# Performance work log

Measured on AMD Instinct MI355X. Metric: run time of the kernel, lower is better.

## Reference

```python
import jax, jax.numpy as jnp
import numpy as np

B, N, NPOINT, NSAMPLE = 8, 8192, 512, 32
D, NHEAD, NLAYERS, DIM_OUT = 128, 8, 4, 256
HD = D // NHEAD
DFF = 2 * D
EPS = 1e-5

_gather = jax.vmap(lambda p, i: p[i])  # p: [N,C], i: [...] -> [...,C]


def _ln(x, g, b):
    m = jnp.mean(x, -1, keepdims=True)
    v = jnp.var(x, -1, keepdims=True)
    return (x - m) / jnp.sqrt(v + EPS) * g + b


def _fps(pts):
    # pts: [B,N,3] -> centroid indices [B,NPOINT]; start index 0 (torch uses randint)
    Bb, Nn, _ = pts.shape
    def step(carry, _):
        dist, far = carry
        cen = jax.vmap(lambda p, f: p[f])(pts, far)[:, None, :]  # [B,1,3]
        dist = jnp.minimum(dist, jnp.sum((pts - cen) ** 2, -1))
        return (dist, jnp.argmax(dist, -1)), far
    init = (jnp.full((Bb, Nn), 1e10, pts.dtype), jnp.zeros((Bb,), jnp.int32))
    _, cents = jax.lax.scan(step, init, None, length=NPOINT)
    return cents.T  # [B,NPOINT]


def _interp_linear(x, n_out):
    # x: [B,C,S] -> [B,C,n_out], linear, align_corners=True
    S = x.shape[-1]
    pos = jnp.arange(n_out) * ((S - 1) / (n_out - 1))
    i0 = jnp.floor(pos).astype(jnp.int32)
    i1 = jnp.minimum(i0 + 1, S - 1)
    w = (pos - i0).astype(x.dtype)
    return x[..., i0] * (1 - w) + x[..., i1] * w


def _layer(x, p):
    wqkv, bqkv, wo, bo, g1, be1, w1, bf1, w2, bf2, g2, be2 = p
    Bt, K, _ = x.shape
    qkv = x @ wqkv.T + bqkv
    q, k, v = jnp.split(qkv, 3, axis=-1)
    q = q.reshape(Bt, K, NHEAD, HD)
    k = k.reshape(Bt, K, NHEAD, HD)
    v = v.reshape(Bt, K, NHEAD, HD)
    att = jax.nn.softmax(jnp.einsum('bqhd,bkhd->bhqk', q, k) / jnp.sqrt(jnp.float32(HD)), axis=-1)
    o = jnp.einsum('bhqk,bkhd->bqhd', att, v).reshape(Bt, K, D)
    x = _ln(x + o @ wo.T + bo, g1, be1)
    ff = jax.nn.relu(x @ w1.T + bf1) @ w2.T + bf2
    return _ln(x + ff, g2, be2)


def setup_inputs():
    key = jax.random.key(0)
    ks = jax.random.split(key, 10)
    w = lambda k, s: jax.random.normal(k, s, jnp.float32) * 0.02
    return {
        'xyz': jax.random.normal(ks[0], (B, 3, N), jnp.float32),
        'features': jax.random.normal(ks[1], (B, D, N), jnp.float32),
        'pe_w1': w(ks[2], (D // 2, 3)), 'pe_b1': jnp.zeros((D // 2,), jnp.float32),
        'bn_gamma': jnp.ones((D // 2,), jnp.float32), 'bn_beta': jnp.zeros((D // 2,), jnp.float32),
        'bn_mean': jnp.zeros((D // 2,), jnp.float32), 'bn_var': jnp.ones((D // 2,), jnp.float32),
        'pe_w2': w(ks[3], (D, D // 2)), 'pe_b2': jnp.zeros((D,), jnp.float32),
        'attn_wqkv': w(ks[4], (NLAYERS, 3 * D, D)), 'attn_bqkv': jnp.zeros((NLAYERS, 3 * D), jnp.float32),
        'attn_wo': w(ks[5], (NLAYERS, D, D)), 'attn_bo': jnp.zeros((NLAYERS, D), jnp.float32),
        'ln1_g': jnp.ones((NLAYERS, D), jnp.float32), 'ln1_b': jnp.zeros((NLAYERS, D), jnp.float32),
        'ffn_w1': w(ks[6], (NLAYERS, DFF, D)), 'ffn_b1': jnp.zeros((NLAYERS, DFF), jnp.float32),
        'ffn_w2': w(ks[7], (NLAYERS, D, DFF)), 'ffn_b2': jnp.zeros((NLAYERS, D), jnp.float32),
        'ln2_g': jnp.ones((NLAYERS, D), jnp.float32), 'ln2_b': jnp.zeros((NLAYERS, D), jnp.float32),
        'fc_w': w(ks[8], (DIM_OUT, D)), 'fc_b': jnp.zeros((DIM_OUT,), jnp.float32),
    }


def reference(xyz, features, pe_w1, pe_b1, bn_gamma, bn_beta, bn_mean, bn_var, pe_w2, pe_b2,
              attn_wqkv, attn_bqkv, attn_wo, attn_bo, ln1_g, ln1_b,
              ffn_w1, ffn_b1, ffn_w2, ffn_b2, ln2_g, ln2_b, fc_w, fc_b):
    pts = jnp.transpose(xyz, (0, 2, 1))                 # [B,N,3]
    fps_idx = _fps(pts)                                 # [B,S]
    new_xyz = _gather(pts, fps_idx)                     # [B,S,3]
    # kNN: squared distances [B,S,N]
    d2 = (jnp.sum(new_xyz ** 2, -1)[..., None] + jnp.sum(pts ** 2, -1)[:, None, :]
          - 2.0 * jnp.einsum('bsc,bnc->bsn', new_xyz, pts))
    _, gidx = jax.lax.top_k(-d2, NSAMPLE)               # [B,S,K]
    gxyz = _gather(pts, gidx)                           # [B,S,K,3]
    gfeat = _gather(jnp.transpose(features, (0, 2, 1)), gidx)  # [B,S,K,D]
    # positional encoding: 1x1 conv -> BN (eval) -> relu -> 1x1 conv
    h = gxyz @ pe_w1.T + pe_b1
    h = (h - bn_mean) / jnp.sqrt(bn_var + EPS) * bn_gamma + bn_beta
    pe = jax.nn.relu(h) @ pe_w2.T + pe_b2               # [B,S,K,D]
    x = (gfeat + pe).reshape(B * NPOINT, NSAMPLE, D)    # tokens: K neighbors per center
    layer_params = (attn_wqkv, attn_bqkv, attn_wo, attn_bo, ln1_g, ln1_b,
                    ffn_w1, ffn_b1, ffn_w2, ffn_b2, ln2_g, ln2_b)
    x, _ = jax.lax.scan(lambda c, p: (_layer(c, p), None), x, layer_params)
    x = x.reshape(B, NPOINT, NSAMPLE, D).max(axis=2)    # max-pool over neighbors [B,S,D]
    out = jnp.transpose(x @ fc_w.T + fc_b, (0, 2, 1))   # [B,DIM_OUT,S]
    out_up = _interp_linear(out, N)                     # [B,DIM_OUT,N]
    return jnp.transpose(new_xyz, (0, 2, 1)), out_up
```

## Files before the change

### kernel.cpp

```cpp
#include <hip/hip_runtime.h>
#include <math.h>

constexpr int CB  = 8;
constexpr int CN  = 8192;
constexpr int CS  = 512;
constexpr int CK  = 32;
constexpr int CD  = 128;
constexpr int CF  = 256;
constexpr int CO  = 256;
constexpr float CEPS = 1e-5f;

typedef __attribute__((ext_vector_type(8)))  short short8;
typedef __attribute__((ext_vector_type(2)))  float f32x2;
typedef __attribute__((ext_vector_type(4)))  float f32x4;
typedef __attribute__((ext_vector_type(16))) float f32x16;
#define MFMA16(a,b,c) __builtin_amdgcn_mfma_f32_16x16x32_bf16(a,b,c,0,0,0)
#define MFMA32(a,b,c) __builtin_amdgcn_mfma_f32_32x32x16_bf16(a,b,c,0,0,0)

__device__ __forceinline__ ushort f2b(float f){
  unsigned u = __builtin_bit_cast(unsigned, f);
  u = u + 0x7fffu + ((u >> 16) & 1u);
  return (ushort)(u >> 16);
}

template<int CTRL, int RM>
__device__ __forceinline__ unsigned long long dpp64(unsigned long long k){
  int lo = (int)(unsigned)k;
  int hi = (int)(unsigned)(k >> 32);
  int plo = __builtin_amdgcn_update_dpp(lo, lo, CTRL, RM, 0xF, false);
  int phi = __builtin_amdgcn_update_dpp(hi, hi, CTRL, RM, 0xF, false);
  return ((unsigned long long)(unsigned)phi << 32) | (unsigned)plo;
}
__device__ __forceinline__ unsigned long long wave_max64(unsigned long long k){
  unsigned long long p;
  p = dpp64<0xB1,0xF>(k); k = p > k ? p : k;
  p = dpp64<0x4E,0xF>(k); k = p > k ? p : k;
  p = dpp64<0x140,0xF>(k); k = p > k ? p : k;
  p = dpp64<0x141,0xF>(k); k = p > k ? p : k;
  p = dpp64<0x142,0xA>(k); k = p > k ? p : k;
  p = dpp64<0x143,0xC>(k); k = p > k ? p : k;
  return k;
}
__device__ __forceinline__ unsigned long long wave_min64(unsigned long long k){
  unsigned long long p;
  p = dpp64<0xB1,0xF>(k); k = p < k ? p : k;
  p = dpp64<0x4E,0xF>(k); k = p < k ? p : k;
  p = dpp64<0x140,0xF>(k); k = p < k ? p : k;
  p = dpp64<0x141,0xF>(k); k = p < k ? p : k;
  p = dpp64<0x142,0xA>(k); k = p < k ? p : k;
  p = dpp64<0x143,0xC>(k); k = p < k ? p : k;
  return k;
}
__device__ __forceinline__ unsigned long long oct_max64(unsigned long long k){
  unsigned long long p;
  p = dpp64<0xB1,0xF>(k); k = p > k ? p : k;
  p = dpp64<0x4E,0xF>(k); k = p > k ? p : k;
  p = dpp64<0x141,0xF>(k); k = p > k ? p : k;
  return k;
}
__device__ __forceinline__ unsigned long long quad_min64(unsigned long long k){
  unsigned long long p;
  p = dpp64<0xB1,0xF>(k); k = p < k ? p : k;
  p = dpp64<0x4E,0xF>(k); k = p < k ? p : k;
  return k;
}

__global__ __launch_bounds__(512)
void fps_fused_kernel(const float* __restrict__ xyz, int* __restrict__ fps_idx,
                      const float* __restrict__ features, float* __restrict__ featT,
                      const float* __restrict__ wqkv, const float* __restrict__ wo,
                      const float* __restrict__ w1,   const float* __restrict__ w2,
                      ushort* __restrict__ wfrag)
{
#pragma clang fp contract(off)
  __shared__ __align__(16) float4 p4[CN];
  __shared__ unsigned long long wred[2][8];
  const int bid = blockIdx.x, t = threadIdx.x;

  if (bid >= CB + 128){
    if (featT == nullptr) return;
    const int tt  = (bid - CB - 128)*2 + (t >> 8);
    const int b2  = tt >> 10;
    const int rem = tt & 1023;
    const int d0  = (rem >> 8) * 32;
    const int n0  = (rem & 255) * 32;
    const int t2  = t & 255;
    const int tx  = t2 & 31, ty = t2 >> 5;
    float* tl = ((float*)p4) + (t >> 8) * (32*33);
    const float* fb = features + (size_t)b2*CD*CN;
    #pragma unroll
    for (int r=0;r<32;r+=8) tl[(ty+r)*33 + tx] = fb[(size_t)(d0+ty+r)*CN + n0+tx];
    __syncthreads();
    float* ftb = featT + (size_t)b2*CN*CD;
    #pragma unroll
    for (int r=0;r<32;r+=8) ftb[(size_t)(n0+ty+r)*CD + d0+tx] = tl[tx*33 + (ty+r)];
    return;
  }
  if (bid >= CB){
    const int tid = (bid - CB)*512 + t;
    const int l = tid & 63;
    const int f = tid >> 6;
    const int L = f >> 8;
    const int r = f & 255;
    const float* src; int stride, nt, kt;
    if (r < 96)      { nt = r>>2;        kt = r&3;        src = wqkv + (size_t)L*384*128; stride = 128; }
    else if (r < 128){ nt = (r-96)>>2;   kt = (r-96)&3;   src = wo   + (size_t)L*128*128; stride = 128; }
    else if (r < 192){ nt = (r-128)>>2;  kt = (r-128)&3;  src = w1   + (size_t)L*256*128; stride = 128; }
    else             { nt = (r-192)>>3;  kt = (r-192)&7;  src = w2   + (size_t)L*128*256; stride = 256; }
    const int n = nt*16 + (l & 15);
    const int k = kt*32 + (l >> 4)*8;
    const float* p = src + (size_t)n*stride + k;
    uint4 o;
    o.x = (unsigned)f2b(p[0]) | ((unsigned)f2b(p[1])<<16);
    o.y = (unsigned)f2b(p[2]) | ((unsigned)f2b(p[3])<<16);
    o.z = (unsigned)f2b(p[4]) | ((unsigned)f2b(p[5])<<16);
    o.w = (unsigned)f2b(p[6]) | ((unsigned)f2b(p[7])<<16);
    *(uint4*)(wfrag + (size_t)tid*8) = o;
    return;
  }

  const int b = bid;
  const int w = t >> 6, lane = t & 63;
  const float* xb = xyz + (size_t)b*3*CN;
  f32x2 px[8], py[8], pz[8], dist[8];
  unsigned ilo[16];
  #pragma unroll
  for (int u=0;u<8;u++){
    const int i0 = t + 512*(2*u);
    const int i1 = t + 512*(2*u+1);
    px[u] = f32x2{xb[i0],      xb[i1]};
    py[u] = f32x2{xb[CN+i0],   xb[CN+i1]};
    pz[u] = f32x2{xb[2*CN+i0], xb[2*CN+i1]};
    dist[u] = f32x2{1e10f, 1e10f};
    ilo[2*u]   = (unsigned)(8191 - i0);
    ilo[2*u+1] = (unsigned)(8191 - i1);
    p4[i0] = make_float4(px[u][0], py[u][0], pz[u][0], 0.f);
    p4[i1] = make_float4(px[u][1], py[u][1], pz[u][1], 0.f);
  }
  __syncthreads();
  int far = 0, par = 0;
  float4 c = p4[0];
  for (int it = 0; it < CS; ++it){
    if (t == 0) fps_idx[b*CS + it] = far;
    unsigned long long kk[16];
    const f32x2 cx2 = {c.x, c.x}, cy2 = {c.y, c.y}, cz2 = {c.z, c.z};
    #pragma unroll
    for (int u=0;u<8;u++){
      const f32x2 dx = px[u] - cx2;
      const f32x2 dy = py[u] - cy2;
      const f32x2 dz = pz[u] - cz2;
      const f32x2 d2 = (dx*dx + dy*dy) + dz*dz;
      const float nd0 = fminf(dist[u][0], d2[0]);
      const float nd1 = fminf(dist[u][1], d2[1]);
      dist[u] = f32x2{nd0, nd1};
      kk[2*u]   = ((unsigned long long)__builtin_bit_cast(unsigned, nd0) << 32) | ilo[2*u];
      kk[2*u+1] = ((unsigned long long)__builtin_bit_cast(unsigned, nd1) << 32) | ilo[2*u+1];
    }
    #pragma unroll
    for (int st=1; st<16; st<<=1)
      #pragma unroll
      for (int j=0;j<16;j+=2*st)
        kk[j] = kk[j] >= kk[j+st] ? kk[j] : kk[j+st];
    const unsigned long long key = wave_max64(kk[0]);
    if (lane == 63) wred[par][w] = key;
    __syncthreads();
    unsigned long long k2 = wred[par][lane & 7];
    k2 = oct_max64(k2);
    far = 8191 - (int)(k2 & 0xFFFFFFFFu);
    c = p4[far];
    par ^= 1;
  }
}

__global__ __launch_bounds__(256)
void knn_kernel(const float* __restrict__ xyz, const int* __restrict__ fps_idx,
                int* __restrict__ gidx, float* __restrict__ out0)
{
#pragma clang fp contract(off)
  __shared__ unsigned long long wredk[2][4];
  const int blk = blockIdx.x, t = threadIdx.x;
  const int w = t >> 6, l = t & 63;
  const int b = blk >> 9;
  const int s = blk & 511;
  const float* xb = xyz + (size_t)b*3*CN;
  const int cidx = fps_idx[b*CS + s];
  const float cx = xb[cidx], cy = xb[CN+cidx], cz = xb[2*CN+cidx];
  const float cn2 = (cx*cx + cy*cy) + cz*cz;
  if (t == 0){
    float* o = out0 + (size_t)b*3*CS + s;
    o[0] = cx; o[CS] = cy; o[2*CS] = cz;
  }
  unsigned long long kv[32];
  #pragma unroll
  for (int j=0;j<32;j++){
    const int i = t + 256*j;
    const float x = xb[i], y = xb[CN+i], z = xb[2*CN+i];
    const float pn2 = (x*x + y*y) + z*z;
    const float dot = (cx*x + cy*y) + cz*z;
    const float d2 = (cn2 + pn2) - 2.0f*dot;
    unsigned u = __builtin_bit_cast(unsigned, d2);
    u ^= (unsigned)((int)u >> 31) | 0x80000000u;
    kv[j] = ((unsigned long long)u << 32) | (unsigned)i;
  }
  unsigned long long mv;
  {
    unsigned long long tmp[16];
    #pragma unroll
    for (int j=0;j<16;j++) tmp[j] = kv[j] < kv[j+16] ? kv[j] : kv[j+16];
    #pragma unroll
    for (int st=8; st>=1; st>>=1)
      #pragma unroll
      for (int j=0;j<st;j++) tmp[j] = tmp[j] < tmp[j+st] ? tmp[j] : tmp[j+st];
    mv = tmp[0];
  }
  int par = 0;
  for (int k=0;k<CK;k++){
    const unsigned long long v = wave_min64(mv);
    if (l == 63) wredk[par][w] = v;
    __syncthreads();
    unsigned long long k2 = wredk[par][l & 3];
    k2 = quad_min64(k2);
    const int win = (int)(k2 & 0xFFFFFFFFu);
    if (t == 0) gidx[(size_t)blk*CK + k] = win;
    if ((win & 255) == t){
      const int jw = win >> 8;
      #pragma unroll
      for (int j=0;j<32;j++) if (j == jw) kv[j] = ~0ull;
      unsigned long long tmp[16];
      #pragma unroll
      for (int j=0;j<16;j++) tmp[j] = kv[j] < kv[j+16] ? kv[j] : kv[j+16];
      #pragma unroll
      for (int st=8; st>=1; st>>=1)
        #pragma unroll
        for (int j=0;j<st;j++) tmp[j] = tmp[j] < tmp[j+st] ? tmp[j] : tmp[j+st];
      mv = tmp[0];
    }
    par ^= 1;
  }
}

__global__ __launch_bounds__(256)
void pe_kernel(const float* __restrict__ xyz, const float* __restrict__ features,
               const float* __restrict__ featT, const int* __restrict__ gidx,
               const float* __restrict__ pe_w1, const float* __restrict__ pe_b1,
               const float* __restrict__ bn_g, const float* __restrict__ bn_b,
               const float* __restrict__ bn_m, const float* __restrict__ bn_v,
               const float* __restrict__ pe_w2, const float* __restrict__ pe_b2,
               float* __restrict__ xout)
{
  __shared__ __align__(16) float w2s[CD*64];
  __shared__ __align__(16) float hr[CK*68];
  __shared__ int idxs[CK];
  __shared__ float gx[CK], gy[CK], gz[CK];
  const int g = blockIdx.x, t = threadIdx.x;
  const int b = g >> 9;
  for (int i=t; i<CD*64; i+=256){
    const int row = i>>6, c = i&63;
    const int u = (c>>2) ^ ((row>>2)&7);
    w2s[row*64 + (u<<2) + (c&3)] = pe_w2[i];
  }
  if (t < CK){
    const int id = gidx[(size_t)g*CK + t];
    idxs[t] = id;
    const float* xb = xyz + (size_t)b*3*CN;
    gx[t] = xb[id]; gy[t] = xb[CN+id]; gz[t] = xb[2*CN+id];
  }
  __syncthreads();
  for (int v=t; v<CK*64; v+=256){
    const int k = v>>6, j = v&63;
    float h = ((gx[k]*pe_w1[j*3] + gy[k]*pe_w1[j*3+1]) + gz[k]*pe_w1[j*3+2]) + pe_b1[j];
    h = (h - bn_m[j]) / sqrtf(bn_v[j] + CEPS) * bn_g[j] + bn_b[j];
    hr[k*68+j] = fmaxf(h, 0.f);
  }
  __syncthreads();
  const int kt = t >> 5, dt = t & 31;
  const int k0 = kt*4, d0 = dt*4;
  const int sw = dt & 7;
  float acc[4][4];
  #pragma unroll
  for (int a=0;a<4;a++)
    #pragma unroll
    for (int bb=0;bb<4;bb++) acc[a][bb] = 0.f;
  for (int j=0;j<16;j++){
    float4 h4[4], w4[4];
    #pragma unroll
    for (int a=0;a<4;a++) h4[a] = *(const float4*)&hr[(k0+a)*68 + j*4];
    #pragma unroll
    for (int bb=0;bb<4;bb++) w4[bb] = *(const float4*)&w2s[(d0+bb)*64 + ((j ^ sw)<<2)];
    #pragma unroll
    for (int a=0;a<4;a++)
      #pragma unroll
      for (int bb=0;bb<4;bb++){
        acc[a][bb] += h4[a].x*w4[bb].x; acc[a][bb] += h4[a].y*w4[bb].y;
        acc[a][bb] += h4[a].z*w4[bb].z; acc[a][bb] += h4[a].w*w4[bb].w;
      }
  }
  const float4 b2v = *(const float4*)&pe_b2[d0];
  const float* fb  = features + (size_t)b*CD*CN;
  const float* ftb = featT ? (featT + (size_t)b*CN*CD) : nullptr;
  #pragma unroll
  for (int a=0;a<4;a++){
    const int id = idxs[k0+a];
    float4 gf;
    if (ftb) gf = *(const float4*)&ftb[(size_t)id*CD + d0];
    else gf = make_float4(fb[(size_t)(d0+0)*CN+id], fb[(size_t)(d0+1)*CN+id],
                          fb[(size_t)(d0+2)*CN+id], fb[(size_t)(d0+3)*CN+id]);
    float4 o;
    o.x = gf.x + (acc[a][0] + b2v.x);
    o.y = gf.y + (acc[a][1] + b2v.y);
    o.z = gf.z + (acc[a][2] + b2v.z);
    o.w = gf.w + (acc[a][3] + b2v.w);
    *(float4*)&xout[(size_t)g*4096 + (size_t)(k0+a)*128 + d0] = o;
  }
}

__device__ __forceinline__ void ln_inplace(float* x32s, ushort* xbv,
                                           const float* __restrict__ gamma,
                                           const float* __restrict__ beta, int t)
{
  const int r = t >> 3, j = t & 7;
  float v[16]; float s = 0.f;
  #pragma unroll
  for (int i=0;i<16;i++){ v[i] = x32s[r*132 + j + 8*i]; s += v[i]; }
  #pragma unroll
  for (int off=1; off<8; off<<=1) s += __shfl_xor(s, off);
  const float mean = s * (1.f/128.f);
  float var = 0.f;
  #pragma unroll
  for (int i=0;i<16;i++){ const float d = v[i]-mean; var += d*d; }
  #pragma unroll
  for (int off=1; off<8; off<<=1) var += __shfl_xor(var, off);
  const float inv = 1.f / sqrtf(var*(1.f/128.f) + CEPS);
  #pragma unroll
  for (int i=0;i<16;i++){
    const int d = j + 8*i;
    const float o = (v[i]-mean)*inv*gamma[d] + beta[d];
    x32s[r*132 + d] = o;
    xbv[r*136 + d] = f2b(o);
  }
}

__global__ __launch_bounds__(256, 2)
void layers_mfma_kernel(const float* __restrict__ xbuf, const ushort* __restrict__ wf,
                        const float* __restrict__ bqkv, const float* __restrict__ bo,
                        const float* __restrict__ g1, const float* __restrict__ b1v,
                        const float* __restrict__ bf1, const float* __restrict__ bf2,
                        const float* __restrict__ g2, const float* __restrict__ b2v,
                        const float* __restrict__ fc_w, const float* __restrict__ fc_b,
                        float* __restrict__ fcout)
{
  __shared__ __align__(16) float  x32s[32*132];
  __shared__ __align__(16) ushort xbv [32*136];
  __shared__ __align__(16) ushort qk  [32*264];
  __shared__ __align__(16) ushort vT  [128*40];
  __shared__ __align__(16) ushort Pb  [4*32*40];
  __shared__ __align__(16) float  pooled[CD];
  const int g = blockIdx.x, t = threadIdx.x;
  const int w = t>>6, l = t&63;
  const int l15 = l&15, q4 = l>>4, l31 = l&31, hi = l>>5;
  const float* xg = xbuf + (size_t)g*1024*4;

  for (int i=t;i<1024;i+=256){
    const float4 v = ((const float4*)xg)[i];
    const int r = i>>5, c = (i&31)*4;
    *(float4*)&x32s[r*132 + c] = v;
    uint2 p;
    p.x = (unsigned)f2b(v.x) | ((unsigned)f2b(v.y)<<16);
    p.y = (unsigned)f2b(v.z) | ((unsigned)f2b(v.w)<<16);
    *(uint2*)&xbv[r*136 + c] = p;
  }
  __syncthreads();

  #pragma unroll 1
  for (int L = 0; L < 4; ++L){
    const uint4*  wfv   = (const uint4*)(wf + (size_t)L*131072);
    const float* bqkvL  = bqkv + (size_t)L*3*CD;
    const float* boL    = bo   + (size_t)L*CD;
    const float* g1L    = g1   + (size_t)L*CD;
    const float* b1L    = b1v  + (size_t)L*CD;
    const float* bf1L   = bf1  + (size_t)L*CF;
    const float* bf2L   = bf2  + (size_t)L*CD;
    const float* g2L    = g2   + (size_t)L*CD;
    const float* b2L    = b2v  + (size_t)L*CD;

    {
      short8 a[2][4];
      #pragma unroll
      for (int mt=0;mt<2;mt++)
        #pragma unroll
        for (int kt=0;kt<4;kt++)
          a[mt][kt] = __builtin_bit_cast(short8, *(const uint4*)&xbv[(l15+16*mt)*136 + kt*32 + q4*8]);
      for (int i=0;i<6;i++){
        const int nt = w + 4*i;
        const int n  = nt*16 + l15;
        f32x4 a0 = {0.f,0.f,0.f,0.f}, a1 = {0.f,0.f,0.f,0.f};
        #pragma unroll
        for (int kt=0;kt<4;kt++){
          const short8 b = __builtin_bit_cast(short8, wfv[(nt*4+kt)*64 + l]);
          a0 = MFMA16(a[0][kt], b, a0);
          a1 = MFMA16(a[1][kt], b, a1);
        }
        const float bias = bqkvL[n];
        if (nt < 16){
          #pragma unroll
          for (int i2=0;i2<4;i2++){
            qk[(q4*4+i2   )*264 + n] = f2b(a0[i2]+bias);
            qk[(q4*4+i2+16)*264 + n] = f2b(a1[i2]+bias);
          }
        } else {
          const int d = n - 256;
          uint2 p0, p1;
          p0.x = (unsigned)f2b(a0[0]+bias) | ((unsigned)f2b(a0[1]+bias)<<16);
          p0.y = (unsigned)f2b(a0[2]+bias) | ((unsigned)f2b(a0[3]+bias)<<16);
          p1.x = (unsigned)f2b(a1[0]+bias) | ((unsigned)f2b(a1[1]+bias)<<16);
          p1.y = (unsigned)f2b(a1[2]+bias) | ((unsigned)f2b(a1[3]+bias)<<16);
          *(uint2*)&vT[d*40 + q4*4]      = p0;
          *(uint2*)&vT[d*40 + 16 + q4*4] = p1;
        }
      }
    }
    __syncthreads();

    for (int hh=0; hh<2; hh++){
      const int h = 2*w + hh;
      const short8 ka = __builtin_bit_cast(short8, *(const uint4*)&qk[l31*264 + 128 + h*16 + hi*8]);
      const short8 qb = __builtin_bit_cast(short8, *(const uint4*)&qk[l31*264 +       h*16 + hi*8]);
      f32x16 s;
      #pragma unroll
      for (int i=0;i<16;i++) s[i] = 0.f;
      s = MFMA32(ka, qb, s);
      float e[16]; float mx = -1e30f;
      #pragma unroll
      for (int i=0;i<16;i++){ e[i] = s[i]*0.25f; mx = fmaxf(mx, e[i]); }
      mx = fmaxf(mx, __shfl_xor(mx, 32));
      float sum = 0.f;
      #pragma unroll
      for (int i=0;i<16;i++){ e[i] = __expf(e[i]-mx); sum += e[i]; }
      sum += __shfl_xor(sum, 32);
      const float inv = 1.f/sum;
      #pragma unroll
      for (int j=0;j<4;j++){
        uint2 p;
        p.x = (unsigned)f2b(e[4*j  ]*inv) | ((unsigned)f2b(e[4*j+1]*inv)<<16);
        p.y = (unsigned)f2b(e[4*j+2]*inv) | ((unsigned)f2b(e[4*j+3]*inv)<<16);
        *(uint2*)&Pb[w*1280 + l31*40 + j*8 + hi*4] = p;
      }
      const short8 bv = __builtin_bit_cast(short8, *(const uint4*)&vT[(h*16+l15)*40 + q4*8]);
      #pragma unroll
      for (int mt=0;mt<2;mt++){
        const short8 ap = __builtin_bit_cast(short8, *(const uint4*)&Pb[w*1280 + (l15+16*mt)*40 + q4*8]);
        f32x4 o = {0.f,0.f,0.f,0.f};
        o = MFMA16(ap, bv, o);
        #pragma unroll
        for (int i2=0;i2<4;i2++)
          xbv[(16*mt + q4*4 + i2)*136 + h*16 + l15] = f2b(o[i2]);
      }
    }
    __syncthreads();

    {
      short8 a[2][4];
      #pragma unroll
      for (int mt=0;mt<2;mt++)
        #pragma unroll
        for (int kt=0;kt<4;kt++)
          a[mt][kt] = __builtin_bit_cast(short8, *(const uint4*)&xbv[(l15+16*mt)*136 + kt*32 + q4*8]);
      for (int i=0;i<2;i++){
        const int nt = w + 4*i;
        const int n  = nt*16 + l15;
        f32x4 a0 = {0.f,0.f,0.f,0.f}, a1 = {0.f,0.f,0.f,0.f};
        #pragma unroll
        for (int kt=0;kt<4;kt++){
          const short8 b = __builtin_bit_cast(short8, wfv[(96 + nt*4+kt)*64 + l]);
          a0 = MFMA16(a[0][kt], b, a0);
          a1 = MFMA16(a[1][kt], b, a1);
        }
        const float bias = boL[n];
        #pragma unroll
        for (int i2=0;i2<4;i2++){
          x32s[(q4*4+i2   )*132 + n] += a0[i2] + bias;
          x32s[(q4*4+i2+16)*132 + n] += a1[i2] + bias;
        }
      }
    }
    __syncthreads();
    ln_inplace(x32s, xbv, g1L, b1L, t);
    __syncthreads();

    {
      short8 a[2][4];
      #pragma unroll
      for (int mt=0;mt<2;mt++)
        #pragma unroll
        for (int kt=0;kt<4;kt++)
          a[mt][kt] = __builtin_bit_cast(short8, *(const uint4*)&xbv[(l15+16*mt)*136 + kt*32 + q4*8]);
      for (int i=0;i<4;i++){
        const int nt = w + 4*i;
        const int n  = nt*16 + l15;
        f32x4 a0 = {0.f,0.f,0.f,0.f}, a1 = {0.f,0.f,0.f,0.f};
        #pragma unroll
        for (int kt=0;kt<4;kt++){
          const short8 b = __builtin_bit_cast(short8, wfv[(128 + nt*4+kt)*64 + l]);
          a0 = MFMA16(a[0][kt], b, a0);
          a1 = MFMA16(a[1][kt], b, a1);
        }
        const float bias = bf1L[n];
        #pragma unroll
        for (int i2=0;i2<4;i2++){
          qk[(q4*4+i2   )*264 + n] = f2b(fmaxf(a0[i2]+bias, 0.f));
          qk[(q4*4+i2+16)*264 + n] = f2b(fmaxf(a1[i2]+bias, 0.f));
        }
      }
    }
    __syncthreads();

    {
      short8 a[2][8];
      #pragma unroll
      for (int mt=0;mt<2;mt++)
        #pragma unroll
        for (int kt=0;kt<8;kt++)
          a[mt][kt] = __builtin_bit_cast(short8, *(const uint4*)&qk[(l15+16*mt)*264 + kt*32 + q4*8]);
      for (int i=0;i<2;i++){
        const int nt = w + 4*i;
        const int n  = nt*16 + l15;
        f32x4 a0 = {0.f,0.f,0.f,0.f}, a1 = {0.f,0.f,0.f,0.f};
        #pragma unroll
        for (int kt=0;kt<8;kt++){
          const short8 b = __builtin_bit_cast(short8, wfv[(192 + nt*8+kt)*64 + l]);
          a0 = MFMA16(a[0][kt], b, a0);
          a1 = MFMA16(a[1][kt], b, a1);
        }
        const float bias = bf2L[n];
        #pragma unroll
        for (int i2=0;i2<4;i2++){
          x32s[(q4*4+i2   )*132 + n] += a0[i2] + bias;
          x32s[(q4*4+i2+16)*132 + n] += a1[i2] + bias;
        }
      }
    }
    __syncthreads();
    ln_inplace(x32s, xbv, g2L, b2L, t);
    __syncthreads();
  }

  if (t < CD){
    float m = -1e30f;
    #pragma unroll
    for (int k=0;k<CK;k++) m = fmaxf(m, x32s[k*132 + t]);
    pooled[t] = m;
  }
  __syncthreads();
  float acc = 0.f;
  const float* wr = fc_w + (size_t)t*CD;
  const float4* pp = (const float4*)pooled;
  #pragma unroll
  for (int i=0;i<CD/4;i++){
    const float4 w4 = *(const float4*)(wr + 4*i);
    const float4 p4 = pp[i];
    acc += p4.x*w4.x; acc += p4.y*w4.y; acc += p4.z*w4.z; acc += p4.w*w4.w;
  }
  acc += fc_b[t];
  const int b = g >> 9, s = g & 511;
  fcout[((size_t)b*CS + s)*CO + t] = acc;
}

__global__ __launch_bounds__(256)
void interp_kernel(const float* __restrict__ fcout, float* __restrict__ out1)
{
  const int idx = blockIdx.x*256 + threadIdx.x;
  const int n  = idx & (CN-1);
  const int bo = idx >> 13;
  const int b  = bo >> 8, o = bo & 255;
  const double pos = (double)n * ((double)(CS-1)/(double)(CN-1));
  const int i0 = (int)pos;
  const int i1 = min(i0+1, CS-1);
  const float w = (float)(pos - (double)i0);
  const float v0 = fcout[((size_t)b*CS + i0)*CO + o];
  const float v1 = fcout[((size_t)b*CS + i1)*CO + o];
  out1[idx] = v0*(1.f - w) + v1*w;
}

extern "C" void kernel_launch(void* const* d_in, const int* in_sizes, int n_in,
                              void* d_out, int out_size, void* d_ws, size_t ws_size,
                              hipStream_t stream)
{
  (void)in_sizes; (void)n_in; (void)out_size;
  const float* xyz      = (const float*)d_in[0];
  const float* features = (const float*)d_in[1];
  const float* pe_w1    = (const float*)d_in[2];
  const float* pe_b1    = (const float*)d_in[3];
  const float* bn_g     = (const float*)d_in[4];
  const float* bn_b     = (const float*)d_in[5];
  const float* bn_m     = (const float*)d_in[6];
  const float* bn_v     = (const float*)d_in[7];
  const float* pe_w2    = (const float*)d_in[8];
  const float* pe_b2    = (const float*)d_in[9];
  const float* wqkv     = (const float*)d_in[10];
  const float* bqkv     = (const float*)d_in[11];
  const float* wo       = (const float*)d_in[12];
  const float* bo       = (const float*)d_in[13];
  const float* g1       = (const float*)d_in[14];
  const float* b1       = (const float*)d_in[15];
  const float* w1       = (const float*)d_in[16];
  const float* bf1      = (const float*)d_in[17];
  const float* w2       = (const float*)d_in[18];
  const float* bf2      = (const float*)d_in[19];
  const float* g2       = (const float*)d_in[20];
  const float* b2       = (const float*)d_in[21];
  const float* fc_w     = (const float*)d_in[22];
  const float* fc_b     = (const float*)d_in[23];

  char* ws = (char*)d_ws;
  int*    fps_idx = (int*)(ws);
  int*    gidx    = (int*)(ws + (16u<<10));
  ushort* wfrag   = (ushort*)(ws + (1u<<20));
  float*  xbuf    = (float*)(ws + (2u<<20));
  float*  fcout   = (float*)(ws + (66u<<20));
  float*  featT   = (float*)(ws + (70u<<20));
  const bool useT = ws_size >= ((size_t)102<<20);

  float* out0 = (float*)d_out;
  float* out1 = out0 + CB*3*CS;

  const int nblk = CB + 128 + (useT ? 4096 : 0);
  fps_fused_kernel<<<nblk, 512, 0, stream>>>(xyz, fps_idx, features,
                                             useT ? featT : nullptr,
                                             wqkv, wo, w1, w2, wfrag);
  knn_kernel<<<CB*CS, 256, 0, stream>>>(xyz, fps_idx, gidx, out0);
  pe_kernel<<<CB*CS, 256, 0, stream>>>(xyz, features, useT ? featT : nullptr, gidx,
                                       pe_w1, pe_b1, bn_g, bn_b, bn_m, bn_v,
                                       pe_w2, pe_b2, xbuf);
  layers_mfma_kernel<<<CB*CS, 256, 0, stream>>>(xbuf, wfrag,
      bqkv, bo, g1, b1, bf1, bf2, g2, b2, fc_w, fc_b, fcout);
  interp_kernel<<<(CB*CO*CN)/256, 256, 0, stream>>>(fcout, out1);
}
```

Baseline: 1.190 ms.

## Pipeline FPS in phases overlapped with KNN, PE and layer work

Splits the serial FPS loop into four launches, each producing 128 centroids and saving the distance state and last index to workspace scratch. Blocks in the same launch process downstream KNN, PE and transformer-layer work for centroids already finished in earlier phases, packing two 256-thread sub-blocks per 512-thread block through a shared-memory union. The remaining tail is handled by the original-style kernels with offsets. The goal is to hide the long single-block-per-batch FPS latency behind the parallel stages. In exchange it adds extra launches, restores the FPS state from global memory each phase, and gives the co-scheduled work blocks the large FPS shared-memory footprint.

Measured after the change: 1.693 ms. 42.3% more time.

```diff
diff --git a/kernel.cpp b/kernel.cpp
--- a/kernel.cpp
+++ b/kernel.cpp
@@ -65,135 +65,69 @@
   return k;
 }
 
-__global__ __launch_bounds__(512)
-void fps_fused_kernel(const float* __restrict__ xyz, int* __restrict__ fps_idx,
-                      const float* __restrict__ features, float* __restrict__ featT,
-                      const float* __restrict__ wqkv, const float* __restrict__ wo,
-                      const float* __restrict__ w1,   const float* __restrict__ w2,
-                      ushort* __restrict__ wfrag)
+struct LayerS {
+  alignas(16) float  x32s[32*132];
+  alignas(16) ushort xbv [32*136];
+  alignas(16) ushort qk  [32*264];
+  alignas(16) ushort vT  [128*40];
+  alignas(16) ushort Pb  [4*32*40];
+  alignas(16) float  pooled[CD];
+};
+struct PeS {
+  alignas(16) float hr[CK*68];
+  int   idxs[CK];
+  float gx[CK], gy[CK], gz[CK];
+};
+union SMem {
+  struct { float4 p4[CN]; unsigned long long wred[2][8]; } fps;
+  struct { LayerS g[2]; } lay;
+  struct { alignas(16) float w2s[CD*64]; PeS g[2]; } pe;
+  struct { float tile[2][32*33]; } tr;
+  struct { unsigned long long wredk[2][2][4]; } knn;
+};
+
+__device__ __forceinline__ void ln_inplace(float* x32s, ushort* xbv,
+                                           const float* __restrict__ gamma,
+                                           const float* __restrict__ beta, int t)
+{
+  const int r = t >> 3, j = t & 7;
+  float v[16]; float s = 0.f;
+  #pragma unroll
+  for (int i=0;i<16;i++){ v[i] = x32s[r*132 + j + 8*i]; s += v[i]; }
+  #pragma unroll
+  for (int off=1; off<8; off<<=1) s += __shfl_xor(s, off);
+  const float mean = s * (1.f/128.f);
+  float var = 0.f;
+  #pragma unroll
+  for (int i=0;i<16;i++){ const float d = v[i]-mean; var += d*d; }
+  #pragma unroll
+  for (int off=1; off<8; off<<=1) var += __shfl_xor(var, off);
+  const float inv = 1.f / sqrtf(var*(1.f/128.f) + CEPS);
+  #pragma unroll
+  for (int i=0;i<16;i++){
+    const int d = j + 8*i;
+    const float o = (v[i]-mean)*inv*gamma[d] + beta[d];
+    x32s[r*132 + d] = o;
+    xbv[r*136 + d] = f2b(o);
+  }
+}
+
+
+__device__ void knn_body(unsigned long long (&wredk)[2][4], const int t2,
+                         const float* __restrict__ xb, const int cidx,
+                         int* __restrict__ gidx_g, float* __restrict__ out0_b, const int s)
 {
 #pragma clang fp contract(off)
-  __shared__ __align__(16) float4 p4[CN];
-  __shared__ unsigned long long wred[2][8];
-  const int bid = blockIdx.x, t = threadIdx.x;
-
-  if (bid >= CB + 128){
-    if (featT == nullptr) return;
-    const int tt  = (bid - CB - 128)*2 + (t >> 8);
-    const int b2  = tt >> 10;
-    const int rem = tt & 1023;
-    const int d0  = (rem >> 8) * 32;
-    const int n0  = (rem & 255) * 32;
-    const int t2  = t & 255;
-    const int tx  = t2 & 31, ty = t2 >> 5;
-    float* tl = ((float*)p4) + (t >> 8) * (32*33);
-    const float* fb = features + (size_t)b2*CD*CN;
-    #pragma unroll
-    for (int r=0;r<32;r+=8) tl[(ty+r)*33 + tx] = fb[(size_t)(d0+ty+r)*CN + n0+tx];
-    __syncthreads();
-    float* ftb = featT + (size_t)b2*CN*CD;
-    #pragma unroll
-    for (int r=0;r<32;r+=8) ftb[(size_t)(n0+ty+r)*CD + d0+tx] = tl[tx*33 + (ty+r)];
-    return;
-  }
-  if (bid >= CB){
-    const int tid = (bid - CB)*512 + t;
-    const int l = tid & 63;
-    const int f = tid >> 6;
-    const int L = f >> 8;
-    const int r = f & 255;
-    const float* src; int stride, nt, kt;
-    if (r < 96)      { nt = r>>2;        kt = r&3;        src = wqkv + (size_t)L*384*128; stride = 128; }
-    else if (r < 128){ nt = (r-96)>>2;   kt = (r-96)&3;   src = wo   + (size_t)L*128*128; stride = 128; }
-    else if (r < 192){ nt = (r-128)>>2;  kt = (r-128)&3;  src = w1   + (size_t)L*256*128; stride = 128; }
-    else             { nt = (r-192)>>3;  kt = (r-192)&7;  src = w2   + (size_t)L*128*256; stride = 256; }
-    const int n = nt*16 + (l & 15);
-    const int k = kt*32 + (l >> 4)*8;
-    const float* p = src + (size_t)n*stride + k;
-    uint4 o;
-    o.x = (unsigned)f2b(p[0]) | ((unsigned)f2b(p[1])<<16);
-    o.y = (unsigned)f2b(p[2]) | ((unsigned)f2b(p[3])<<16);
-    o.z = (unsigned)f2b(p[4]) | ((unsigned)f2b(p[5])<<16);
-    o.w = (unsigned)f2b(p[6]) | ((unsigned)f2b(p[7])<<16);
-    *(uint4*)(wfrag + (size_t)tid*8) = o;
-    return;
-  }
-
-  const int b = bid;
-  const int w = t >> 6, lane = t & 63;
-  const float* xb = xyz + (size_t)b*3*CN;
-  f32x2 px[8], py[8], pz[8], dist[8];
-  unsigned ilo[16];
-  #pragma unroll
-  for (int u=0;u<8;u++){
-    const int i0 = t + 512*(2*u);
-    const int i1 = t + 512*(2*u+1);
-    px[u] = f32x2{xb[i0],      xb[i1]};
-    py[u] = f32x2{xb[CN+i0],   xb[CN+i1]};
-    pz[u] = f32x2{xb[2*CN+i0], xb[2*CN+i1]};
-    dist[u] = f32x2{1e10f, 1e10f};
-    ilo[2*u]   = (unsigned)(8191 - i0);
-    ilo[2*u+1] = (unsigned)(8191 - i1);
-    p4[i0] = make_float4(px[u][0], py[u][0], pz[u][0], 0.f);
-    p4[i1] = make_float4(px[u][1], py[u][1], pz[u][1], 0.f);
-  }
-  __syncthreads();
-  int far = 0, par = 0;
-  float4 c = p4[0];
-  for (int it = 0; it < CS; ++it){
-    if (t == 0) fps_idx[b*CS + it] = far;
-    unsigned long long kk[16];
-    const f32x2 cx2 = {c.x, c.x}, cy2 = {c.y, c.y}, cz2 = {c.z, c.z};
-    #pragma unroll
-    for (int u=0;u<8;u++){
-      const f32x2 dx = px[u] - cx2;
-      const f32x2 dy = py[u] - cy2;
-      const f32x2 dz = pz[u] - cz2;
-      const f32x2 d2 = (dx*dx + dy*dy) + dz*dz;
-      const float nd0 = fminf(dist[u][0], d2[0]);
-      const float nd1 = fminf(dist[u][1], d2[1]);
-      dist[u] = f32x2{nd0, nd1};
-      kk[2*u]   = ((unsigned long long)__builtin_bit_cast(unsigned, nd0) << 32) | ilo[2*u];
-      kk[2*u+1] = ((unsigned long long)__builtin_bit_cast(unsigned, nd1) << 32) | ilo[2*u+1];
-    }
-    #pragma unroll
-    for (int st=1; st<16; st<<=1)
-      #pragma unroll
-      for (int j=0;j<16;j+=2*st)
-        kk[j] = kk[j] >= kk[j+st] ? kk[j] : kk[j+st];
-    const unsigned long long key = wave_max64(kk[0]);
-    if (lane == 63) wred[par][w] = key;
-    __syncthreads();
-    unsigned long long k2 = wred[par][lane & 7];
-    k2 = oct_max64(k2);
-    far = 8191 - (int)(k2 & 0xFFFFFFFFu);
-    c = p4[far];
-    par ^= 1;
-  }
-}
-
-__global__ __launch_bounds__(256)
-void knn_kernel(const float* __restrict__ xyz, const int* __restrict__ fps_idx,
-                int* __restrict__ gidx, float* __restrict__ out0)
-{
-#pragma clang fp contract(off)
-  __shared__ unsigned long long wredk[2][4];
-  const int blk = blockIdx.x, t = threadIdx.x;
-  const int w = t >> 6, l = t & 63;
-  const int b = blk >> 9;
-  const int s = blk & 511;
-  const float* xb = xyz + (size_t)b*3*CN;
-  const int cidx = fps_idx[b*CS + s];
+  const int w = t2 >> 6, l = t2 & 63;
   const float cx = xb[cidx], cy = xb[CN+cidx], cz = xb[2*CN+cidx];
   const float cn2 = (cx*cx + cy*cy) + cz*cz;
-  if (t == 0){
-    float* o = out0 + (size_t)b*3*CS + s;
-    o[0] = cx; o[CS] = cy; o[2*CS] = cz;
+  if (t2 == 0){
+    out0_b[s] = cx; out0_b[CS+s] = cy; out0_b[2*CS+s] = cz;
   }
   unsigned long long kv[32];
   #pragma unroll
   for (int j=0;j<32;j++){
-    const int i = t + 256*j;
+    const int i = t2 + 256*j;
     const float x = xb[i], y = xb[CN+i], z = xb[2*CN+i];
     const float pn2 = (x*x + y*y) + z*z;
     const float dot = (cx*x + cy*y) + cz*z;
@@ -221,8 +155,8 @@
     unsigned long long k2 = wredk[par][l & 3];
     k2 = quad_min64(k2);
     const int win = (int)(k2 & 0xFFFFFFFFu);
-    if (t == 0) gidx[(size_t)blk*CK + k] = win;
-    if ((win & 255) == t){
+    if (t2 == 0) gidx_g[k] = win;
+    if ((win & 255) == t2){
       const int jw = win >> 8;
       #pragma unroll
       for (int j=0;j<32;j++) if (j == jw) kv[j] = ~0ull;
@@ -239,41 +173,31 @@
   }
 }
 
-__global__ __launch_bounds__(256)
-void pe_kernel(const float* __restrict__ xyz, const float* __restrict__ features,
-               const float* __restrict__ featT, const int* __restrict__ gidx,
-               const float* __restrict__ pe_w1, const float* __restrict__ pe_b1,
-               const float* __restrict__ bn_g, const float* __restrict__ bn_b,
-               const float* __restrict__ bn_m, const float* __restrict__ bn_v,
-               const float* __restrict__ pe_w2, const float* __restrict__ pe_b2,
-               float* __restrict__ xout)
-{
-  __shared__ __align__(16) float w2s[CD*64];
-  __shared__ __align__(16) float hr[CK*68];
-  __shared__ int idxs[CK];
-  __shared__ float gx[CK], gy[CK], gz[CK];
-  const int g = blockIdx.x, t = threadIdx.x;
-  const int b = g >> 9;
-  for (int i=t; i<CD*64; i+=256){
-    const int row = i>>6, c = i&63;
-    const int u = (c>>2) ^ ((row>>2)&7);
-    w2s[row*64 + (u<<2) + (c&3)] = pe_w2[i];
-  }
-  if (t < CK){
-    const int id = gidx[(size_t)g*CK + t];
-    idxs[t] = id;
+__device__ void pe_body(const float* __restrict__ w2s, PeS& P, const int t2,
+                        const int b, const int g,
+                        const float* __restrict__ xyz,
+                        const float* __restrict__ features, const float* __restrict__ featT,
+                        const int* __restrict__ gidx,
+                        const float* __restrict__ pe_w1, const float* __restrict__ pe_b1,
+                        const float* __restrict__ bn_g, const float* __restrict__ bn_b,
+                        const float* __restrict__ bn_m, const float* __restrict__ bn_v,
+                        const float* __restrict__ pe_b2, float* __restrict__ xout)
+{
+  if (t2 < CK){
+    const int id = gidx[(size_t)g*CK + t2];
+    P.idxs[t2] = id;
     const float* xb = xyz + (size_t)b*3*CN;
-    gx[t] = xb[id]; gy[t] = xb[CN+id]; gz[t] = xb[2*CN+id];
+    P.gx[t2] = xb[id]; P.gy[t2] = xb[CN+id]; P.gz[t2] = xb[2*CN+id];
   }
   __syncthreads();
-  for (int v=t; v<CK*64; v+=256){
+  for (int v=t2; v<CK*64; v+=256){
     const int k = v>>6, j = v&63;
-    float h = ((gx[k]*pe_w1[j*3] + gy[k]*pe_w1[j*3+1]) + gz[k]*pe_w1[j*3+2]) + pe_b1[j];
+    float h = ((P.gx[k]*pe_w1[j*3] + P.gy[k]*pe_w1[j*3+1]) + P.gz[k]*pe_w1[j*3+2]) + pe_b1[j];
     h = (h - bn_m[j]) / sqrtf(bn_v[j] + CEPS) * bn_g[j] + bn_b[j];
-    hr[k*68+j] = fmaxf(h, 0.f);
+    P.hr[k*68+j] = fmaxf(h, 0.f);
   }
   __syncthreads();
-  const int kt = t >> 5, dt = t & 31;
+  const int kt = t2 >> 5, dt = t2 & 31;
   const int k0 = kt*4, d0 = dt*4;
   const int sw = dt & 7;
   float acc[4][4];
@@ -284,7 +208,7 @@
   for (int j=0;j<16;j++){
     float4 h4[4], w4[4];
     #pragma unroll
-    for (int a=0;a<4;a++) h4[a] = *(const float4*)&hr[(k0+a)*68 + j*4];
+    for (int a=0;a<4;a++) h4[a] = *(const float4*)&P.hr[(k0+a)*68 + j*4];
     #pragma unroll
     for (int bb=0;bb<4;bb++) w4[bb] = *(const float4*)&w2s[(d0+bb)*64 + ((j ^ sw)<<2)];
     #pragma unroll
@@ -300,7 +224,7 @@
   const float* ftb = featT ? (featT + (size_t)b*CN*CD) : nullptr;
   #pragma unroll
   for (int a=0;a<4;a++){
-    const int id = idxs[k0+a];
+    const int id = P.idxs[k0+a];
     float4 gf;
     if (ftb) gf = *(const float4*)&ftb[(size_t)id*CD + d0];
     else gf = make_float4(fb[(size_t)(d0+0)*CN+id], fb[(size_t)(d0+1)*CN+id],
@@ -314,66 +238,32 @@
   }
 }
 
-__device__ __forceinline__ void ln_inplace(float* x32s, ushort* xbv,
-                                           const float* __restrict__ gamma,
-                                           const float* __restrict__ beta, int t)
-{
-  const int r = t >> 3, j = t & 7;
-  float v[16]; float s = 0.f;
-  #pragma unroll
-  for (int i=0;i<16;i++){ v[i] = x32s[r*132 + j + 8*i]; s += v[i]; }
-  #pragma unroll
-  for (int off=1; off<8; off<<=1) s += __shfl_xor(s, off);
-  const float mean = s * (1.f/128.f);
-  float var = 0.f;
-  #pragma unroll
-  for (int i=0;i<16;i++){ const float d = v[i]-mean; var += d*d; }
-  #pragma unroll
-  for (int off=1; off<8; off<<=1) var += __shfl_xor(var, off);
-  const float inv = 1.f / sqrtf(var*(1.f/128.f) + CEPS);
-  #pragma unroll
-  for (int i=0;i<16;i++){
-    const int d = j + 8*i;
-    const float o = (v[i]-mean)*inv*gamma[d] + beta[d];
-    x32s[r*132 + d] = o;
-    xbv[r*136 + d] = f2b(o);
-  }
-}
-
-__global__ __launch_bounds__(256, 2)
-void layers_mfma_kernel(const float* __restrict__ xbuf, const ushort* __restrict__ wf,
-                        const float* __restrict__ bqkv, const float* __restrict__ bo,
-                        const float* __restrict__ g1, const float* __restrict__ b1v,
-                        const float* __restrict__ bf1, const float* __restrict__ bf2,
-                        const float* __restrict__ g2, const float* __restrict__ b2v,
-                        const float* __restrict__ fc_w, const float* __restrict__ fc_b,
-                        float* __restrict__ fcout)
-{
-  __shared__ __align__(16) float  x32s[32*132];
-  __shared__ __align__(16) ushort xbv [32*136];
-  __shared__ __align__(16) ushort qk  [32*264];
-  __shared__ __align__(16) ushort vT  [128*40];
-  __shared__ __align__(16) ushort Pb  [4*32*40];
-  __shared__ __align__(16) float  pooled[CD];
-  const int g = blockIdx.x, t = threadIdx.x;
-  const int w = t>>6, l = t&63;
+__device__ void layers_body(LayerS& S, const int t2, const float* __restrict__ xg,
+                            const ushort* __restrict__ wf,
+                            const float* __restrict__ bqkv, const float* __restrict__ bo,
+                            const float* __restrict__ g1, const float* __restrict__ b1v,
+                            const float* __restrict__ bf1, const float* __restrict__ bf2,
+                            const float* __restrict__ g2, const float* __restrict__ b2v,
+                            const float* __restrict__ fc_w, const float* __restrict__ fc_b,
+                            float* __restrict__ fcout, const int b, const int s)
+{
+  const int w = t2>>6, l = t2&63;
   const int l15 = l&15, q4 = l>>4, l31 = l&31, hi = l>>5;
-  const float* xg = xbuf + (size_t)g*1024*4;
-
-  for (int i=t;i<1024;i+=256){
+
+  for (int i=t2;i<1024;i+=256){
     const float4 v = ((const float4*)xg)[i];
     const int r = i>>5, c = (i&31)*4;
-    *(float4*)&x32s[r*132 + c] = v;
+    *(float4*)&S.x32s[r*132 + c] = v;
     uint2 p;
     p.x = (unsigned)f2b(v.x) | ((unsigned)f2b(v.y)<<16);
     p.y = (unsigned)f2b(v.z) | ((unsigned)f2b(v.w)<<16);
-    *(uint2*)&xbv[r*136 + c] = p;
+    *(uint2*)&S.xbv[r*136 + c] = p;
   }
   __syncthreads();
 
   #pragma unroll 1
   for (int L = 0; L < 4; ++L){
-    const uint4*  wfv   = (const uint4*)(wf + (size_t)L*131072);
+    const uint4* wfv    = (const uint4*)(wf + (size_t)L*131072);
     const float* bqkvL  = bqkv + (size_t)L*3*CD;
     const float* boL    = bo   + (size_t)L*CD;
     const float* g1L    = g1   + (size_t)L*CD;
@@ -389,23 +279,23 @@
       for (int mt=0;mt<2;mt++)
         #pragma unroll
         for (int kt=0;kt<4;kt++)
-          a[mt][kt] = __builtin_bit_cast(short8, *(const uint4*)&xbv[(l15+16*mt)*136 + kt*32 + q4*8]);
+          a[mt][kt] = __builtin_bit_cast(short8, *(const uint4*)&S.xbv[(l15+16*mt)*136 + kt*32 + q4*8]);
       for (int i=0;i<6;i++){
         const int nt = w + 4*i;
         const int n  = nt*16 + l15;
         f32x4 a0 = {0.f,0.f,0.f,0.f}, a1 = {0.f,0.f,0.f,0.f};
         #pragma unroll
         for (int kt=0;kt<4;kt++){
-          const short8 b = __builtin_bit_cast(short8, wfv[(nt*4+kt)*64 + l]);
-          a0 = MFMA16(a[0][kt], b, a0);
-          a1 = MFMA16(a[1][kt], b, a1);
+          const short8 bb = __builtin_bit_cast(short8, wfv[(nt*4+kt)*64 + l]);
+          a0 = MFMA16(a[0][kt], bb, a0);
+          a1 = MFMA16(a[1][kt], bb, a1);
         }
         const float bias = bqkvL[n];
         if (nt < 16){
           #pragma unroll
           for (int i2=0;i2<4;i2++){
-            qk[(q4*4+i2   )*264 + n] = f2b(a0[i2]+bias);
-            qk[(q4*4+i2+16)*264 + n] = f2b(a1[i2]+bias);
+            S.qk[(q4*4+i2   )*264 + n] = f2b(a0[i2]+bias);
+            S.qk[(q4*4+i2+16)*264 + n] = f2b(a1[i2]+bias);
           }
         } else {
           const int d = n - 256;
@@ -414,24 +304,24 @@
           p0.y = (unsigned)f2b(a0[2]+bias) | ((unsigned)f2b(a0[3]+bias)<<16);
           p1.x = (unsigned)f2b(a1[0]+bias) | ((unsigned)f2b(a1[1]+bias)<<16);
           p1.y = (unsigned)f2b(a1[2]+bias) | ((unsigned)f2b(a1[3]+bias)<<16);
-          *(uint2*)&vT[d*40 + q4*4]      = p0;
-          *(uint2*)&vT[d*40 + 16 + q4*4] = p1;
+          *(uint2*)&S.vT[d*40 + q4*4]      = p0;
+          *(uint2*)&S.vT[d*40 + 16 + q4*4] = p1;
         }
       }
     }
     __syncthreads();
 
     for (int hh=0; hh<2; hh++){
-      const int h = 2*w + hh;
-      const short8 ka = __builtin_bit_cast(short8, *(const uint4*)&qk[l31*264 + 128 + h*16 + hi*8]);
-      const short8 qb = __builtin_bit_cast(short8, *(const uint4*)&qk[l31*264 +       h*16 + hi*8]);
-      f32x16 s;
-      #pragma unroll
-      for (int i=0;i<16;i++) s[i] = 0.f;
-      s = MFMA32(ka, qb, s);
+      const int hd = 2*w + hh;
+      const short8 ka = __builtin_bit_cast(short8, *(const uint4*)&S.qk[l31*264 + 128 + hd*16 + hi*8]);
+      const short8 qb = __builtin_bit_cast(short8, *(const uint4*)&S.qk[l31*264 +       hd*16 + hi*8]);
+      f32x16 sreg;
+      #pragma unroll
+      for (int i=0;i<16;i++) sreg[i] = 0.f;
+      sreg = MFMA32(ka, qb, sreg);
       float e[16]; float mx = -1e30f;
       #pragma unroll
-      for (int i=0;i<16;i++){ e[i] = s[i]*0.25f; mx = fmaxf(mx, e[i]); }
+      for (int i=0;i<16;i++){ e[i] = sreg[i]*0.25f; mx = fmaxf(mx, e[i]); }
       mx = fmaxf(mx, __shfl_xor(mx, 32));
       float sum = 0.f;
       #pragma unroll
@@ -443,17 +333,17 @@
         uint2 p;
         p.x = (unsigned)f2b(e[4*j  ]*inv) | ((unsigned)f2b(e[4*j+1]*inv)<<16);
         p.y = (unsigned)f2b(e[4*j+2]*inv) | ((unsigned)f2b(e[4*j+3]*inv)<<16);
-        *(uint2*)&Pb[w*1280 + l31*40 + j*8 + hi*4] = p;
-      }
-      const short8 bv = __builtin_bit_cast(short8, *(const uint4*)&vT[(h*16+l15)*40 + q4*8]);
+        *(uint2*)&S.Pb[w*1280 + l31*40 + j*8 + hi*4] = p;
+      }
+      const short8 bv = __builtin_bit_cast(short8, *(const uint4*)&S.vT[(hd*16+l15)*40 + q4*8]);
       #pragma unroll
       for (int mt=0;mt<2;mt++){
-        const short8 ap = __builtin_bit_cast(short8, *(const uint4*)&Pb[w*1280 + (l15+16*mt)*40 + q4*8]);
+        const short8 ap = __builtin_bit_cast(short8, *(const uint4*)&S.Pb[w*1280 + (l15+16*mt)*40 + q4*8]);
         f32x4 o = {0.f,0.f,0.f,0.f};
         o = MFMA16(ap, bv, o);
         #pragma unroll
         for (int i2=0;i2<4;i2++)
-          xbv[(16*mt + q4*4 + i2)*136 + h*16 + l15] = f2b(o[i2]);
+          S.xbv[(16*mt + q4*4 + i2)*136 + hd*16 + l15] = f2b(o[i2]);
       }
     }
     __syncthreads();
@@ -464,27 +354,27 @@
       for (int mt=0;mt<2;mt++)
         #pragma unroll
         for (int kt=0;kt<4;kt++)
-          a[mt][kt] = __builtin_bit_cast(short8, *(const uint4*)&xbv[(l15+16*mt)*136 + kt*32 + q4*8]);
+          a[mt][kt] = __builtin_bit_cast(short8, *(const uint4*)&S.xbv[(l15+16*mt)*136 + kt*32 + q4*8]);
       for (int i=0;i<2;i++){
         const int nt = w + 4*i;
         const int n  = nt*16 + l15;
         f32x4 a0 = {0.f,0.f,0.f,0.f}, a1 = {0.f,0.f,0.f,0.f};
         #pragma unroll
         for (int kt=0;kt<4;kt++){
-          const short8 b = __builtin_bit_cast(short8, wfv[(96 + nt*4+kt)*64 + l]);
-          a0 = MFMA16(a[0][kt], b, a0);
-          a1 = MFMA16(a[1][kt], b, a1);
+          const short8 bb = __builtin_bit_cast(short8, wfv[(96 + nt*4+kt)*64 + l]);
+          a0 = MFMA16(a[0][kt], bb, a0);
+          a1 = MFMA16(a[1][kt], bb, a1);
         }
         const float bias = boL[n];
         #pragma unroll
         for (int i2=0;i2<4;i2++){
-          x32s[(q4*4+i2   )*132 + n] += a0[i2] + bias;
-          x32s[(q4*4+i2+16)*132 + n] += a1[i2] + bias;
+          S.x32s[(q4*4+i2   )*132 + n] += a0[i2] + bias;
+          S.x32s[(q4*4+i2+16)*132 + n] += a1[i2] + bias;
         }
       }
     }
     __syncthreads();
-    ln_inplace(x32s, xbv, g1L, b1L, t);
+    ln_inplace(S.x32s, S.xbv, g1L, b1L, t2);
     __syncthreads();
 
     {
@@ -493,22 +383,22 @@
       for (int mt=0;mt<2;mt++)
         #pragma unroll
         for (int kt=0;kt<4;kt++)
-          a[mt][kt] = __builtin_bit_cast(short8, *(const uint4*)&xbv[(l15+16*mt)*136 + kt*32 + q4*8]);
+          a[mt][kt] = __builtin_bit_cast(short8, *(const uint4*)&S.xbv[(l15+16*mt)*136 + kt*32 + q4*8]);
       for (int i=0;i<4;i++){
         const int nt = w + 4*i;
         const int n  = nt*16 + l15;
         f32x4 a0 = {0.f,0.f,0.f,0.f}, a1 = {0.f,0.f,0.f,0.f};
         #pragma unroll
         for (int kt=0;kt<4;kt++){
-          const short8 b = __builtin_bit_cast(short8, wfv[(128 + nt*4+kt)*64 + l]);
-          a0 = MFMA16(a[0][kt], b, a0);
-          a1 = MFMA16(a[1][kt], b, a1);
+          const short8 bb = __builtin_bit_cast(short8, wfv[(128 + nt*4+kt)*64 + l]);
+          a0 = MFMA16(a[0][kt], bb, a0);
+          a1 = MFMA16(a[1][kt], bb, a1);
         }
         const float bias = bf1L[n];
         #pragma unroll
         for (int i2=0;i2<4;i2++){
-          qk[(q4*4+i2   )*264 + n] = f2b(fmaxf(a0[i2]+bias, 0.f));
-          qk[(q4*4+i2+16)*264 + n] = f2b(fmaxf(a1[i2]+bias, 0.f));
+          S.qk[(q4*4+i2   )*264 + n] = f2b(fmaxf(a0[i2]+bias, 0.f));
+          S.qk[(q4*4+i2+16)*264 + n] = f2b(fmaxf(a1[i2]+bias, 0.f));
         }
       }
     }
@@ -520,49 +410,268 @@
       for (int mt=0;mt<2;mt++)
         #pragma unroll
         for (int kt=0;kt<8;kt++)
-          a[mt][kt] = __builtin_bit_cast(short8, *(const uint4*)&qk[(l15+16*mt)*264 + kt*32 + q4*8]);
+          a[mt][kt] = __builtin_bit_cast(short8, *(const uint4*)&S.qk[(l15+16*mt)*264 + kt*32 + q4*8]);
       for (int i=0;i<2;i++){
         const int nt = w + 4*i;
         const int n  = nt*16 + l15;
         f32x4 a0 = {0.f,0.f,0.f,0.f}, a1 = {0.f,0.f,0.f,0.f};
         #pragma unroll
         for (int kt=0;kt<8;kt++){
-          const short8 b = __builtin_bit_cast(short8, wfv[(192 + nt*8+kt)*64 + l]);
-          a0 = MFMA16(a[0][kt], b, a0);
-          a1 = MFMA16(a[1][kt], b, a1);
+          const short8 bb = __builtin_bit_cast(short8, wfv[(192 + nt*8+kt)*64 + l]);
+          a0 = MFMA16(a[0][kt], bb, a0);
+          a1 = MFMA16(a[1][kt], bb, a1);
         }
         const float bias = bf2L[n];
         #pragma unroll
         for (int i2=0;i2<4;i2++){
-          x32s[(q4*4+i2   )*132 + n] += a0[i2] + bias;
-          x32s[(q4*4+i2+16)*132 + n] += a1[i2] + bias;
+          S.x32s[(q4*4+i2   )*132 + n] += a0[i2] + bias;
+          S.x32s[(q4*4+i2+16)*132 + n] += a1[i2] + bias;
         }
       }
     }
     __syncthreads();
-    ln_inplace(x32s, xbv, g2L, b2L, t);
-    __syncthreads();
-  }
-
-  if (t < CD){
+    ln_inplace(S.x32s, S.xbv, g2L, b2L, t2);
+    __syncthreads();
+  }
+
+  if (t2 < CD){
     float m = -1e30f;
     #pragma unroll
-    for (int k=0;k<CK;k++) m = fmaxf(m, x32s[k*132 + t]);
-    pooled[t] = m;
+    for (int k=0;k<CK;k++) m = fmaxf(m, S.x32s[k*132 + t2]);
+    S.pooled[t2] = m;
   }
   __syncthreads();
   float acc = 0.f;
-  const float* wr = fc_w + (size_t)t*CD;
-  const float4* pp = (const float4*)pooled;
+  const float* wr = fc_w + (size_t)t2*CD;
+  const float4* pp = (const float4*)S.pooled;
   #pragma unroll
   for (int i=0;i<CD/4;i++){
     const float4 w4 = *(const float4*)(wr + 4*i);
-    const float4 p4 = pp[i];
-    acc += p4.x*w4.x; acc += p4.y*w4.y; acc += p4.z*w4.z; acc += p4.w*w4.w;
-  }
-  acc += fc_b[t];
-  const int b = g >> 9, s = g & 511;
-  fcout[((size_t)b*CS + s)*CO + t] = acc;
+    const float4 p4v = pp[i];
+    acc += p4v.x*w4.x; acc += p4v.y*w4.y; acc += p4v.z*w4.z; acc += p4v.w*w4.w;
+  }
+  acc += fc_b[t2];
+  fcout[((size_t)b*CS + s)*CO + t2] = acc;
+  __syncthreads();
+}
+
+__global__ __launch_bounds__(512, 2)
+void pipe_kernel(const int phase,
+                 const float* __restrict__ xyz, int* __restrict__ fps_idx,
+                 int* __restrict__ fscr, float* __restrict__ dscr,
+                 const float* __restrict__ features, float* __restrict__ featT,
+                 const float* __restrict__ wqkv, const float* __restrict__ wo,
+                 const float* __restrict__ w1,   const float* __restrict__ w2,
+                 ushort* __restrict__ wfrag,
+                 const float* __restrict__ pe_w1, const float* __restrict__ pe_b1,
+                 const float* __restrict__ bn_g, const float* __restrict__ bn_b,
+                 const float* __restrict__ bn_m, const float* __restrict__ bn_v,
+                 const float* __restrict__ pe_w2, const float* __restrict__ pe_b2,
+                 int* __restrict__ gidx, float* __restrict__ xbuf, float* __restrict__ out0,
+                 const float* __restrict__ bqkv, const float* __restrict__ bo,
+                 const float* __restrict__ g1, const float* __restrict__ b1v,
+                 const float* __restrict__ bf1, const float* __restrict__ bf2,
+                 const float* __restrict__ g2, const float* __restrict__ b2v,
+                 const float* __restrict__ fc_w, const float* __restrict__ fc_b,
+                 float* __restrict__ fcout)
+{
+  __shared__ SMem sm;
+  const int bid = blockIdx.x, t = threadIdx.x;
+
+  if (bid < CB){
+#pragma clang fp contract(off)
+    const int b = bid;
+    const int w = t >> 6, lane = t & 63;
+    const float* xb = xyz + (size_t)b*3*CN;
+    float* db = dscr + (size_t)b*CN;
+    f32x2 px[8], py[8], pz[8], dist[8];
+    unsigned ilo[16];
+    #pragma unroll
+    for (int u=0;u<8;u++){
+      const int i0 = t + 512*(2*u);
+      const int i1 = t + 512*(2*u+1);
+      px[u] = f32x2{xb[i0],      xb[i1]};
+      py[u] = f32x2{xb[CN+i0],   xb[CN+i1]};
+      pz[u] = f32x2{xb[2*CN+i0], xb[2*CN+i1]};
+      if (phase == 0) dist[u] = f32x2{1e10f, 1e10f};
+      else            dist[u] = f32x2{db[i0], db[i1]};
+      ilo[2*u]   = (unsigned)(8191 - i0);
+      ilo[2*u+1] = (unsigned)(8191 - i1);
+      sm.fps.p4[i0] = make_float4(px[u][0], py[u][0], pz[u][0], 0.f);
+      sm.fps.p4[i1] = make_float4(px[u][1], py[u][1], pz[u][1], 0.f);
+    }
+    __syncthreads();
+    int far = (phase == 0) ? 0 : fscr[b];
+    int par = 0;
+    float4 c = sm.fps.p4[far];
+    const int it0 = phase*128, it1 = it0 + 128;
+    for (int it = it0; it < it1; ++it){
+      if (t == 0) fps_idx[b*CS + it] = far;
+      unsigned long long kk[16];
+      const f32x2 cx2 = {c.x, c.x}, cy2 = {c.y, c.y}, cz2 = {c.z, c.z};
+      #pragma unroll
+      for (int u=0;u<8;u++){
+        const f32x2 dx = px[u] - cx2;
+        const f32x2 dy = py[u] - cy2;
+        const f32x2 dz = pz[u] - cz2;
+        const f32x2 d2 = (dx*dx + dy*dy) + dz*dz;
+        const float nd0 = fminf(dist[u][0], d2[0]);
+        const float nd1 = fminf(dist[u][1], d2[1]);
+        dist[u] = f32x2{nd0, nd1};
+        kk[2*u]   = ((unsigned long long)__builtin_bit_cast(unsigned, nd0) << 32) | ilo[2*u];
+        kk[2*u+1] = ((unsigned long long)__builtin_bit_cast(unsigned, nd1) << 32) | ilo[2*u+1];
+      }
+      #pragma unroll
+      for (int st=1; st<16; st<<=1)
+        #pragma unroll
+        for (int j=0;j<16;j+=2*st)
+          kk[j] = kk[j] >= kk[j+st] ? kk[j] : kk[j+st];
+      const unsigned long long key = wave_max64(kk[0]);
+      if (lane == 63) sm.fps.wred[par][w] = key;
+      __syncthreads();
+      unsigned long long k2 = sm.fps.wred[par][lane & 7];
+      k2 = oct_max64(k2);
+      far = 8191 - (int)(k2 & 0xFFFFFFFFu);
+      c = sm.fps.p4[far];
+      par ^= 1;
+    }
+    if (phase < 3){
+      #pragma unroll
+      for (int u=0;u<8;u++){
+        const int i0 = t + 512*(2*u), i1 = t + 512*(2*u+1);
+        db[i0] = dist[u][0]; db[i1] = dist[u][1];
+      }
+      if (t == 0) fscr[b] = far;
+    }
+    return;
+  }
+
+  if (phase == 0){
+    if (bid < CB + 128){
+      const int tid = (bid - CB)*512 + t;
+      const int l = tid & 63;
+      const int f = tid >> 6;
+      const int L = f >> 8;
+      const int r = f & 255;
+      const float* src; int stride, nt, kt;
+      if (r < 96)      { nt = r>>2;        kt = r&3;        src = wqkv + (size_t)L*384*128; stride = 128; }
+      else if (r < 128){ nt = (r-96)>>2;   kt = (r-96)&3;   src = wo   + (size_t)L*128*128; stride = 128; }
+      else if (r < 192){ nt = (r-128)>>2;  kt = (r-128)&3;  src = w1   + (size_t)L*256*128; stride = 128; }
+      else             { nt = (r-192)>>3;  kt = (r-192)&7;  src = w2   + (size_t)L*128*256; stride = 256; }
+      const int n = nt*16 + (l & 15);
+      const int k = kt*32 + (l >> 4)*8;
+      const float* p = src + (size_t)n*stride + k;
+      uint4 o;
+      o.x = (unsigned)f2b(p[0]) | ((unsigned)f2b(p[1])<<16);
+      o.y = (unsigned)f2b(p[2]) | ((unsigned)f2b(p[3])<<16);
+      o.z = (unsigned)f2b(p[4]) | ((unsigned)f2b(p[5])<<16);
+      o.w = (unsigned)f2b(p[6]) | ((unsigned)f2b(p[7])<<16);
+      *(uint4*)(wfrag + (size_t)tid*8) = o;
+    } else {
+      if (featT == nullptr) return;
+      const int tt  = (bid - CB - 128)*2 + (t >> 8);
+      const int b2  = tt >> 10;
+      const int rem = tt & 1023;
+      const int d0  = (rem >> 8) * 32;
+      const int n0  = (rem & 255) * 32;
+      const int t2_ = t & 255;
+      const int tx  = t2_ & 31, ty = t2_ >> 5;
+      float* tl = sm.tr.tile[t >> 8];
+      const float* fb = features + (size_t)b2*CD*CN;
+      #pragma unroll
+      for (int r=0;r<32;r+=8) tl[(ty+r)*33 + tx] = fb[(size_t)(d0+ty+r)*CN + n0+tx];
+      __syncthreads();
+      float* ftb = featT + (size_t)b2*CN*CD;
+      #pragma unroll
+      for (int r=0;r<32;r+=8) ftb[(size_t)(n0+ty+r)*CD + d0+tx] = tl[tx*33 + (ty+r)];
+    }
+    return;
+  }
+
+  const int rb = bid - CB;
+  const int h = t >> 8, t2 = t & 255;
+  if (rb < 512){
+    const int u = (phase-1)*1024 + rb*2 + h;
+    const int b = u & 7, s = u >> 3;
+    const int g = b*512 + s;
+    const float* xb = xyz + (size_t)b*3*CN;
+    knn_body(sm.knn.wredk[h], t2, xb, fps_idx[b*CS + s],
+             gidx + (size_t)g*CK, out0 + (size_t)b*3*CS, s);
+    return;
+  }
+  if (rb < 1024){
+    for (int i=t; i<CD*64; i+=512){
+      const int row = i>>6, cc = i&63;
+      const int uu = (cc>>2) ^ ((row>>2)&7);
+      sm.pe.w2s[row*64 + (uu<<2) + (cc&3)] = pe_w2[i];
+    }
+    const int u = (phase-2)*1024 + (rb-512)*2 + h;
+    const int b = u & 7, s = u >> 3;
+    const int g = b*512 + s;
+    pe_body(sm.pe.w2s, sm.pe.g[h], t2, b, g, xyz, features, featT, gidx,
+            pe_w1, pe_b1, bn_g, bn_b, bn_m, bn_v, pe_b2, xbuf);
+    return;
+  }
+  {
+    const int u = (rb-1024)*2 + h;
+    const int b = u & 7, s = u >> 3;
+    const int g = b*512 + s;
+    layers_body(sm.lay.g[h], t2, xbuf + (size_t)g*4096, wfrag,
+                bqkv, bo, g1, b1v, bf1, bf2, g2, b2v, fc_w, fc_b, fcout, b, s);
+  }
+}
+
+__global__ __launch_bounds__(256)
+void knn_kernel(const float* __restrict__ xyz, const int* __restrict__ fps_idx,
+                int* __restrict__ gidx, float* __restrict__ out0, const int u0)
+{
+  __shared__ unsigned long long wredk[2][4];
+  const int u = u0 + blockIdx.x;
+  const int b = u & 7, s = u >> 3;
+  const int g = b*512 + s;
+  knn_body(wredk, threadIdx.x, xyz + (size_t)b*3*CN, fps_idx[b*CS + s],
+           gidx + (size_t)g*CK, out0 + (size_t)b*3*CS, s);
+}
+
+__global__ __launch_bounds__(256)
+void pe_kernel(const float* __restrict__ xyz, const float* __restrict__ features,
+               const float* __restrict__ featT, const int* __restrict__ gidx,
+               const float* __restrict__ pe_w1, const float* __restrict__ pe_b1,
+               const float* __restrict__ bn_g, const float* __restrict__ bn_b,
+               const float* __restrict__ bn_m, const float* __restrict__ bn_v,
+               const float* __restrict__ pe_w2, const float* __restrict__ pe_b2,
+               float* __restrict__ xout, const int u0)
+{
+  __shared__ __align__(16) float w2s[CD*64];
+  __shared__ PeS P;
+  const int t = threadIdx.x;
+  for (int i=t; i<CD*64; i+=256){
+    const int row = i>>6, cc = i&63;
+    const int uu = (cc>>2) ^ ((row>>2)&7);
+    w2s[row*64 + (uu<<2) + (cc&3)] = pe_w2[i];
+  }
+  const int u = u0 + blockIdx.x;
+  const int b = u & 7, s = u >> 3;
+  const int g = b*512 + s;
+  pe_body(w2s, P, t, b, g, xyz, features, featT, gidx,
+          pe_w1, pe_b1, bn_g, bn_b, bn_m, bn_v, pe_b2, xout);
+}
+
+__global__ __launch_bounds__(256, 2)
+void layers_mfma_kernel(const float* __restrict__ xbuf, const ushort* __restrict__ wf,
+                        const float* __restrict__ bqkv, const float* __restrict__ bo,
+                        const float* __restrict__ g1, const float* __restrict__ b1v,
+                        const float* __restrict__ bf1, const float* __restrict__ bf2,
+                        const float* __restrict__ g2, const float* __restrict__ b2v,
+                        const float* __restrict__ fc_w, const float* __restrict__ fc_b,
+                        float* __restrict__ fcout, const int u0)
+{
+  __shared__ LayerS S;
+  const int u = u0 + blockIdx.x;
+  const int b = u & 7, s = u >> 3;
+  const int g = b*512 + s;
+  layers_body(S, threadIdx.x, xbuf + (size_t)g*4096, wf,
+              bqkv, bo, g1, b1v, bf1, bf2, g2, b2v, fc_w, fc_b, fcout, b, s);
 }
 
 __global__ __launch_bounds__(256)
@@ -614,6 +723,8 @@
   char* ws = (char*)d_ws;
   int*    fps_idx = (int*)(ws);
   int*    gidx    = (int*)(ws + (16u<<10));
+  int*    fscr    = (int*)(ws + (544u<<10));
+  float*  dscr    = (float*)(ws + (576u<<10));
   ushort* wfrag   = (ushort*)(ws + (1u<<20));
   float*  xbuf    = (float*)(ws + (2u<<20));
   float*  fcout   = (float*)(ws + (66u<<20));
@@ -623,15 +734,23 @@
   float* out0 = (float*)d_out;
   float* out1 = out0 + CB*3*CS;
 
-  const int nblk = CB + 128 + (useT ? 4096 : 0);
-  fps_fused_kernel<<<nblk, 512, 0, stream>>>(xyz, fps_idx, features,
-                                             useT ? featT : nullptr,
-                                             wqkv, wo, w1, w2, wfrag);
-  knn_kernel<<<CB*CS, 256, 0, stream>>>(xyz, fps_idx, gidx, out0);
-  pe_kernel<<<CB*CS, 256, 0, stream>>>(xyz, features, useT ? featT : nullptr, gidx,
-                                       pe_w1, pe_b1, bn_g, bn_b, bn_m, bn_v,
-                                       pe_w2, pe_b2, xbuf);
-  layers_mfma_kernel<<<CB*CS, 256, 0, stream>>>(xbuf, wfrag,
-      bqkv, bo, g1, b1, bf1, bf2, g2, b2, fc_w, fc_b, fcout);
+  for (int p = 0; p < 4; ++p){
+    int grid;
+    if (p == 0)      grid = CB + 128 + (useT ? 4096 : 0);
+    else if (p == 1) grid = CB + 512;
+    else if (p == 2) grid = CB + 1024;
+    else             grid = CB + 1280;
+    pipe_kernel<<<grid, 512, 0, stream>>>(p, xyz, fps_idx, fscr, dscr,
+        features, useT ? featT : nullptr, wqkv, wo, w1, w2, wfrag,
+        pe_w1, pe_b1, bn_g, bn_b, bn_m, bn_v, pe_w2, pe_b2,
+        gidx, xbuf, out0,
+        bqkv, bo, g1, b1, bf1, bf2, g2, b2, fc_w, fc_b, fcout);
+  }
+  knn_kernel<<<1024, 256, 0, stream>>>(xyz, fps_idx, gidx, out0, 3072);
+  pe_kernel<<<2048, 256, 0, stream>>>(xyz, features, useT ? featT : nullptr, gidx,
+                                      pe_w1, pe_b1, bn_g, bn_b, bn_m, bn_v,
+                                      pe_w2, pe_b2, xbuf, 2048);
+  layers_mfma_kernel<<<3584, 256, 0, stream>>>(xbuf, wfrag,
+      bqkv, bo, g1, b1, bf1, bf2, g2, b2, fc_w, fc_b, fcout, 512);
   interp_kernel<<<(CB*CO*CN)/256, 256, 0, stream>>>(fcout, out1);
 }
```
